# Kernel optimization log

Hardware: AMD Instinct MI355X
Metric: run time of the kernel (lower is better)

## Reference

```python
import jax, jax.numpy as jnp
import numpy as np

S, B, I, H = 512, 64, 512, 512

def setup_inputs() -> dict:
    key = jax.random.key(0)
    ks = jax.random.split(key, 10)
    inp = {
        'x':    jax.random.normal(ks[0], (S, B, I), dtype=jnp.float32),
        'W_xi': jax.random.normal(ks[1], (H, I), dtype=jnp.float32) * (1.0 / np.sqrt(I)),
        'W_hi': jax.random.normal(ks[2], (H, H), dtype=jnp.float32) * (1.0 / np.sqrt(H)),
        'b_i':  jax.random.normal(ks[3], (H,), dtype=jnp.float32),
        'W_xc': jax.random.normal(ks[4], (H, I), dtype=jnp.float32) * (1.0 / np.sqrt(I)),
        'W_hc': jax.random.normal(ks[5], (H, H), dtype=jnp.float32) * (1.0 / np.sqrt(H)),
        'b_c':  jax.random.normal(ks[6], (H,), dtype=jnp.float32),
        'W_xo': jax.random.normal(ks[7], (H, I), dtype=jnp.float32) * (1.0 / np.sqrt(I)),
        'W_ho': jax.random.normal(ks[8], (H, H), dtype=jnp.float32) * (1.0 / np.sqrt(H)),
        'b_o':  jax.random.normal(ks[9], (H,), dtype=jnp.float32),
    }
    return inp

def reference(x, W_xi, W_hi, b_i, W_xc, W_hc, b_c, W_xo, W_ho, b_o):
    seq_len, batch, _ = x.shape
    hidden = W_hi.shape[0]
    # Precompute all input-to-gate projections in one pass: [S,B,H] each
    xi = jnp.einsum('sbi,hi->sbh', x, W_xi)
    xc = jnp.einsum('sbi,hi->sbh', x, W_xc)
    xo = jnp.einsum('sbi,hi->sbh', x, W_xo)

    h0 = jnp.zeros((batch, hidden), dtype=x.dtype)
    c0 = jnp.zeros((batch, hidden), dtype=x.dtype)

    def step(carry, xs):
        h, c = carry
        xi_t, xc_t, xo_t = xs
        i_t = jax.nn.sigmoid(xi_t + h @ W_hi.T + b_i)
        c_hat = jnp.tanh(xc_t + h @ W_hc.T + b_c)
        c = (1.0 - i_t) * c + i_t * c_hat  # coupled forget gate f = 1 - i
        o_t = jax.nn.sigmoid(xo_t + h @ W_ho.T + b_o)
        h = o_t * jnp.tanh(c)
        return (h, c), h

    (h_t, c_t), output = jax.lax.scan(step, (h0, c0), (xi, xc, xo))
    # output: [S,B,H] (time-major, matching torch after transposes)
    return output, h_t, c_t
```

## Files before the change

### kernel.cpp

```cpp
#include <hip/hip_runtime.h>
#include <math.h>

#define SEQ   512
#define BATCH 64
#define HID   512
#define NROW  1536
#define XROW_FLOATS ((size_t)SEQ * NROW * BATCH)
#define HBUF_QWORDS (2 * BATCH * HID)
#define SBH ((size_t)SEQ * BATCH * HID)

__device__ __forceinline__ float sigf(float x) {
    return 1.f / (1.f + __expf(-x));
}
__device__ __forceinline__ float tanh_fast(float x) {
    float ax = fabsf(x);
    float e = __expf(-2.f * ax);
    float r = (1.f - e) / (1.f + e);
    return copysignf(r, x);
}
template <int CTRL>
__device__ __forceinline__ float dpp_add(float v) {
    int x = __builtin_amdgcn_update_dpp(0, __builtin_bit_cast(int, v),
                                        CTRL, 0xf, 0xf, true);
    return v + __builtin_bit_cast(float, x);
}

__global__ __launch_bounds__(256) void xproj_kernel(
    const float* __restrict__ x, const float* __restrict__ Wxi,
    const float* __restrict__ Wxc, const float* __restrict__ Wxo,
    float* __restrict__ xrow)
{
    extern __shared__ float lds[];
    float* xT = lds;
    const int tid = threadIdx.x, lane = tid & 63, wv = tid >> 6;
    float* wl = lds + 256 * 65 + wv * (8 * 256);
    const int t = blockIdx.x;

    for (int kh = 0; kh < 2; ++kh) {
        __syncthreads();
        for (int b = wv; b < 64; b += 4) {
            const float* xp = x + ((size_t)t * 64 + b) * 512 + kh * 256;
            #pragma unroll
            for (int q = 0; q < 4; ++q) {
                int k = lane + q * 64;
                xT[k * 65 + b] = xp[k];
            }
        }
        __syncthreads();

        for (int m = 0; m < 48; ++m) {
            const int Bk = wv + 4 * m;
            const int R0 = Bk * 8;
            #pragma unroll
            for (int r = 0; r < 8; ++r) {
                const int R = R0 + r, g = R >> 9, j = R & 511;
                const float* wsrc = (g == 0) ? Wxi : ((g == 1) ? Wxc : Wxo);
                const float4 w4 = *(const float4*)(wsrc + (size_t)j * 512 + kh * 256 + lane * 4);
                *(float4*)(wl + r * 256 + lane * 4) = w4;
            }
            float acc[8] = {0.f, 0.f, 0.f, 0.f, 0.f, 0.f, 0.f, 0.f};
            #pragma unroll 2
            for (int c = 0; c < 64; ++c) {
                const float x0 = xT[(4 * c + 0) * 65 + lane];
                const float x1 = xT[(4 * c + 1) * 65 + lane];
                const float x2 = xT[(4 * c + 2) * 65 + lane];
                const float x3 = xT[(4 * c + 3) * 65 + lane];
                #pragma unroll
                for (int r = 0; r < 8; ++r) {
                    const float4 w4 = *(const float4*)(wl + r * 256 + c * 4);
                    acc[r] += x0 * w4.x + x1 * w4.y + x2 * w4.z + x3 * w4.w;
                }
            }
            #pragma unroll
            for (int r = 0; r < 8; ++r) {
                const size_t o = ((size_t)t * NROW + R0 + r) * 64 + lane;
                if (kh) xrow[o] += acc[r];
                else    xrow[o]  = acc[r];
            }
        }
    }
}

#define WPAD 52
#define HPAD 12
#define W_FLOATS (512 * WPAD)
#define H_FLOATS (512 * HPAD)
__global__ __launch_bounds__(384) void scan_kernel(
    const float* __restrict__ xrow,
    const float* __restrict__ Whi, const float* __restrict__ Whc, const float* __restrict__ Who,
    const float* __restrict__ bi, const float* __restrict__ bc, const float* __restrict__ bo,
    unsigned long long* __restrict__ hbuf, float* __restrict__ out)
{
    extern __shared__ float lds[];
    float* wlds = lds;
    float* hlds = lds + W_FLOATS;
    float* gbuf = lds + W_FLOATS + H_FLOATS;
    float* biasL = gbuf + 384;

    const int tid = threadIdx.x, lane = tid & 63;
    const int gid = blockIdx.x & 7;
    const int m   = blockIdx.x >> 3;
    const int rg  = tid >> 5, ks = tid & 31;

    for (int idx = tid; idx < 48 * 512; idx += 384) {
        const int rho = idx >> 9, k = idx & 511;
        const int g = rho >> 4, jloc = rho & 15;
        const float* wsrc = (g == 0) ? Whi : ((g == 1) ? Whc : Who);
        wlds[k * WPAD + rho] = wsrc[(size_t)(m * 16 + jloc) * 512 + k];
    }
    if (tid < 48) {
        const int g = tid >> 4, jloc = tid & 15;
        const float* bb = (g == 0) ? bi : ((g == 1) ? bc : bo);
        biasL[tid] = bb[m * 16 + jloc];
    }

    const int ejl = tid & 15, eb = tid >> 4;
    const int jg  = m * 16 + ejl;
    const int bg  = gid * 8 + eb;
    float creg = 0.f;

    if (tid < 128) hlds[jg * HPAD + eb] = 0.f;
    __syncthreads();

    for (int t = 0; t < SEQ; ++t) {
        float xr0 = 0.f, xr1 = 0.f, xr2 = 0.f;
        if (tid < 128) {
            const size_t base = ((size_t)t * NROW + jg) * 64 + bg;
            xr0 = xrow[base];
            xr1 = xrow[base + (size_t)512 * 64];
            xr2 = xrow[base + (size_t)1024 * 64];
        }

        {
            const unsigned long long* hsrc =
                hbuf + (size_t)(t & 1) * (BATCH * HID) + (size_t)gid * 8 * 512;
            const unsigned tgt = (unsigned)t;
            unsigned long long hv[11];
            unsigned pend = 0;
            #pragma unroll
            for (int q = 0; q < 11; ++q) {
                const int i = tid + q * 384;
                if (i < 4096 && ((i & 511) >> 4) != m) {
                    hv[q] = __hip_atomic_load(hsrc + i, __ATOMIC_RELAXED,
                                              __HIP_MEMORY_SCOPE_AGENT);
                    pend |= 1u << q;
                }
            }
            while (pend) {
                unsigned np = 0;
                #pragma unroll
                for (int q = 0; q < 11; ++q) {
                    if ((pend >> q) & 1) {
                        const int i = tid + q * 384;
                        if ((unsigned)(hv[q] >> 32) >= tgt) {
                            hlds[(i & 511) * HPAD + (i >> 9)] =
                                __builtin_bit_cast(float, (unsigned)hv[q]);
                        } else np |= 1u << q;
                    }
                }
                if (np) {
                    __builtin_amdgcn_s_sleep(1);
                    #pragma unroll
                    for (int q = 0; q < 11; ++q)
                        if ((np >> q) & 1)
                            hv[q] = __hip_atomic_load(hsrc + (tid + q * 384),
                                                      __ATOMIC_RELAXED,
                                                      __HIP_MEMORY_SCOPE_AGENT);
                }
                pend = np;
            }
        }
        __syncthreads();

        float acc[4][8];
        #pragma unroll
        for (int r = 0; r < 4; ++r)
            #pragma unroll
            for (int b = 0; b < 8; ++b) acc[r][b] = 0.f;

        if (rg < 12) {
            const float* wb = wlds + ks * WPAD + rg * 4;
            const float* hb = hlds + ks * HPAD;
            #pragma unroll
            for (int i = 0; i < 16; ++i) {
                float wv[4], hv2[8];
                *(float4*)&wv[0]  = *(const float4*)(wb + i * (32 * WPAD));
                *(float4*)&hv2[0] = *(const float4*)(hb + i * (32 * HPAD));
                *(float4*)&hv2[4] = *(const float4*)(hb + i * (32 * HPAD) + 4);
                #pragma unroll
                for (int r = 0; r < 4; ++r)
                    #pragma unroll
                    for (int b = 0; b < 8; ++b)
                        acc[r][b] += wv[r] * hv2[b];
            }
            #pragma unroll
            for (int r = 0; r < 4; ++r)
                #pragma unroll
                for (int b = 0; b < 8; ++b) {
                    float v = acc[r][b];
                    v = dpp_add<0x121>(v);
                    v = dpp_add<0x122>(v);
                    v = dpp_add<0x124>(v);
                    v = dpp_add<0x128>(v);
                    v = dpp_add<0x142>(v);
                    acc[r][b] = v;
                }
            if (lane == 16 || lane == 48) {
                #pragma unroll
                for (int r = 0; r < 4; ++r) {
                    float* gp = gbuf + (rg * 4 + r) * 8;
                    *(float4*)gp       = make_float4(acc[r][0], acc[r][1], acc[r][2], acc[r][3]);
                    *(float4*)(gp + 4) = make_float4(acc[r][4], acc[r][5], acc[r][6], acc[r][7]);
                }
            }
        }
        __syncthreads();

        if (tid < 128) {
            const float pi = xr0 + biasL[ejl]      + gbuf[(0 * 16 + ejl) * 8 + eb];
            const float pc = xr1 + biasL[16 + ejl] + gbuf[(1 * 16 + ejl) * 8 + eb];
            const float po = xr2 + biasL[32 + ejl] + gbuf[(2 * 16 + ejl) * 8 + eb];
            const float it = sigf(pi);
            const float ch = tanh_fast(pc);
            const float ot = sigf(po);
            creg = (1.f - it) * creg + it * ch;
            const float hn = ot * tanh_fast(creg);
            const unsigned long long pv =
                ((unsigned long long)(unsigned)(t + 1) << 32) |
                (unsigned long long)__builtin_bit_cast(unsigned, hn);
            __hip_atomic_store(hbuf + (size_t)((t + 1) & 1) * (BATCH * HID)
                                    + (size_t)bg * 512 + jg,
                               pv, __ATOMIC_RELAXED, __HIP_MEMORY_SCOPE_AGENT);
            hlds[jg * HPAD + eb] = hn;
            out[((size_t)t * 64 + bg) * 512 + jg] = hn;
            if (t == SEQ - 1) {
                out[SBH + (size_t)bg * 512 + jg] = hn;
                out[SBH + 32768 + (size_t)bg * 512 + jg] = creg;
            }
        }
    }
}

extern "C" void kernel_launch(void* const* d_in, const int* in_sizes, int n_in,
                              void* d_out, int out_size, void* d_ws, size_t ws_size,
                              hipStream_t stream)
{
    const float* x   = (const float*)d_in[0];
    const float* Wxi = (const float*)d_in[1];
    const float* Whi = (const float*)d_in[2];
    const float* bi  = (const float*)d_in[3];
    const float* Wxc = (const float*)d_in[4];
    const float* Whc = (const float*)d_in[5];
    const float* bc  = (const float*)d_in[6];
    const float* Wxo = (const float*)d_in[7];
    const float* Who = (const float*)d_in[8];
    const float* bo  = (const float*)d_in[9];
    float* out = (float*)d_out;
    char* ws = (char*)d_ws;

    float*              xrow = (float*)ws;
    unsigned long long* hbuf = (unsigned long long*)(ws + XROW_FLOATS * 4);

    (void)hipMemsetAsync(hbuf, 0, (size_t)HBUF_QWORDS * 8, stream);

    hipLaunchKernelGGL(xproj_kernel, dim3(512), dim3(256), 99328, stream,
                       x, Wxi, Wxc, Wxo, xrow);
    hipLaunchKernelGGL(scan_kernel, dim3(256), dim3(384), 132800, stream,
                       xrow, Whi, Whc, Who, bi, bc, bo, hbuf, out);
}
```

Baseline: 4.946 ms.

## Keep recurrent weights in registers and read input weights directly from global

The scan kernel now loads each thread's slice of the recurrent weights into registers once, instead of staging them in LDS. This removes per-step LDS weight reads and cuts LDS use sharply. H padding drops to 10 floats and is read as float2. The x-projection kernel drops its LDS weight staging and reads weights from global/L1, with launch bounds asking for 2 blocks per CU. Also, the poll-loop sleep now comes after the reissued loads. The risks are register pressure from 64 extra weight registers and uncoalesced per-lane global weight reads in xproj.

```diff
diff --git a/kernel.cpp b/kernel.cpp
--- a/kernel.cpp
+++ b/kernel.cpp
@@ -25,7 +25,7 @@
     return v + __builtin_bit_cast(float, x);
 }
 
-__global__ __launch_bounds__(256) void xproj_kernel(
+__global__ __launch_bounds__(256, 2) void xproj_kernel(
     const float* __restrict__ x, const float* __restrict__ Wxi,
     const float* __restrict__ Wxc, const float* __restrict__ Wxo,
     float* __restrict__ xrow)
@@ -33,7 +33,6 @@
     extern __shared__ float lds[];
     float* xT = lds;
     const int tid = threadIdx.x, lane = tid & 63, wv = tid >> 6;
-    float* wl = lds + 256 * 65 + wv * (8 * 256);
     const int t = blockIdx.x;
 
     for (int kh = 0; kh < 2; ++kh) {
@@ -49,14 +48,13 @@
         __syncthreads();
 
         for (int m = 0; m < 48; ++m) {
-            const int Bk = wv + 4 * m;
-            const int R0 = Bk * 8;
+            const int R0 = (wv + 4 * m) * 8;
+            const float* wr[8];
             #pragma unroll
             for (int r = 0; r < 8; ++r) {
                 const int R = R0 + r, g = R >> 9, j = R & 511;
                 const float* wsrc = (g == 0) ? Wxi : ((g == 1) ? Wxc : Wxo);
-                const float4 w4 = *(const float4*)(wsrc + (size_t)j * 512 + kh * 256 + lane * 4);
-                *(float4*)(wl + r * 256 + lane * 4) = w4;
+                wr[r] = wsrc + (size_t)j * 512 + kh * 256;
             }
             float acc[8] = {0.f, 0.f, 0.f, 0.f, 0.f, 0.f, 0.f, 0.f};
             #pragma unroll 2
@@ -67,7 +65,7 @@
                 const float x3 = xT[(4 * c + 3) * 65 + lane];
                 #pragma unroll
                 for (int r = 0; r < 8; ++r) {
-                    const float4 w4 = *(const float4*)(wl + r * 256 + c * 4);
+                    const float4 w4 = *(const float4*)(wr[r] + 4 * c);
                     acc[r] += x0 * w4.x + x1 * w4.y + x2 * w4.z + x3 * w4.w;
                 }
             }
@@ -81,9 +79,7 @@
     }
 }
 
-#define WPAD 52
-#define HPAD 12
-#define W_FLOATS (512 * WPAD)
+#define HPAD 10
 #define H_FLOATS (512 * HPAD)
 __global__ __launch_bounds__(384) void scan_kernel(
     const float* __restrict__ xrow,
@@ -92,9 +88,8 @@
     unsigned long long* __restrict__ hbuf, float* __restrict__ out)
 {
     extern __shared__ float lds[];
-    float* wlds = lds;
-    float* hlds = lds + W_FLOATS;
-    float* gbuf = lds + W_FLOATS + H_FLOATS;
+    float* hlds = lds;
+    float* gbuf = lds + H_FLOATS;
     float* biasL = gbuf + 384;
 
     const int tid = threadIdx.x, lane = tid & 63;
@@ -102,11 +97,17 @@
     const int m   = blockIdx.x >> 3;
     const int rg  = tid >> 5, ks = tid & 31;
 
-    for (int idx = tid; idx < 48 * 512; idx += 384) {
-        const int rho = idx >> 9, k = idx & 511;
-        const int g = rho >> 4, jloc = rho & 15;
+    float w4r[16][4];
+    {
+        const int g  = rg >> 2;
+        const int jb = m * 16 + (rg & 3) * 4;
         const float* wsrc = (g == 0) ? Whi : ((g == 1) ? Whc : Who);
-        wlds[k * WPAD + rho] = wsrc[(size_t)(m * 16 + jloc) * 512 + k];
+        #pragma unroll
+        for (int r = 0; r < 4; ++r) {
+            const float* wp = wsrc + (size_t)(jb + r) * 512 + ks;
+            #pragma unroll
+            for (int i = 0; i < 16; ++i) w4r[i][r] = wp[32 * i];
+        }
     }
     if (tid < 48) {
         const int g = tid >> 4, jloc = tid & 15;
@@ -159,13 +160,13 @@
                     }
                 }
                 if (np) {
-                    __builtin_amdgcn_s_sleep(1);
                     #pragma unroll
                     for (int q = 0; q < 11; ++q)
                         if ((np >> q) & 1)
                             hv[q] = __hip_atomic_load(hsrc + (tid + q * 384),
                                                       __ATOMIC_RELAXED,
                                                       __HIP_MEMORY_SCOPE_AGENT);
+                    __builtin_amdgcn_s_sleep(1);
                 }
                 pend = np;
             }
@@ -178,20 +179,20 @@
             #pragma unroll
             for (int b = 0; b < 8; ++b) acc[r][b] = 0.f;
 
-        if (rg < 12) {
-            const float* wb = wlds + ks * WPAD + rg * 4;
+        {
             const float* hb = hlds + ks * HPAD;
             #pragma unroll
             for (int i = 0; i < 16; ++i) {
-                float wv[4], hv2[8];
-                *(float4*)&wv[0]  = *(const float4*)(wb + i * (32 * WPAD));
-                *(float4*)&hv2[0] = *(const float4*)(hb + i * (32 * HPAD));
-                *(float4*)&hv2[4] = *(const float4*)(hb + i * (32 * HPAD) + 4);
+                float hv2[8];
+                *(float2*)&hv2[0] = *(const float2*)(hb + i * (32 * HPAD) + 0);
+                *(float2*)&hv2[2] = *(const float2*)(hb + i * (32 * HPAD) + 2);
+                *(float2*)&hv2[4] = *(const float2*)(hb + i * (32 * HPAD) + 4);
+                *(float2*)&hv2[6] = *(const float2*)(hb + i * (32 * HPAD) + 6);
                 #pragma unroll
                 for (int r = 0; r < 4; ++r)
                     #pragma unroll
                     for (int b = 0; b < 8; ++b)
-                        acc[r][b] += wv[r] * hv2[b];
+                        acc[r][b] += w4r[i][r] * hv2[b];
             }
             #pragma unroll
             for (int r = 0; r < 4; ++r)
@@ -263,8 +264,8 @@
 
     (void)hipMemsetAsync(hbuf, 0, (size_t)HBUF_QWORDS * 8, stream);
 
-    hipLaunchKernelGGL(xproj_kernel, dim3(512), dim3(256), 99328, stream,
+    hipLaunchKernelGGL(xproj_kernel, dim3(512), dim3(256), 66560, stream,
                        x, Wxi, Wxc, Wxo, xrow);
-    hipLaunchKernelGGL(scan_kernel, dim3(256), dim3(384), 132800, stream,
+    hipLaunchKernelGGL(scan_kernel, dim3(256), dim3(384), 22208, stream,
                        xrow, Whi, Whc, Who, bi, bc, bo, hbuf, out);
 }
```

Result: slower. 6.934 ms (+40.2%).
